# Performance work log

Hardware: AMD Instinct MI355X
Metric: run time of the kernel (lower is better)

The kernel has to match this reference:

```python
import jax, jax.numpy as jnp
import numpy as np

B, T, D = 16, 1024, 256
H, DK = 2, 128          # n_head, d_k = d_v = D // n_head
K = 5                   # conv kernel size
TEMP = float(np.sqrt(D))  # temperature = d_model ** 0.5


def mish(x):
    return x * jnp.tanh(jax.nn.softplus(x))


def setup_inputs() -> dict:
    key = jax.random.key(0)
    ks = jax.random.split(key, 16)
    s = 0.02
    p = lambda k, shp: jax.random.normal(k, shp, dtype=jnp.float32) * s
    inp = {
        'x': jax.random.normal(ks[0], (B, T, D), dtype=jnp.float32),
        'mask': jax.random.randint(ks[1], (B, T), 0, 2).astype(bool),
        # spectral MLP
        'W1': p(ks[2], (D, D)), 'b1': p(ks[3], (D,)),
        'W2': p(ks[4], (D, D)), 'b2': p(ks[5], (D,)),
        # two Conv1dGLU blocks: Conv1d(D -> 2D, k=5), torch layout [out,in,k]
        'cW1': p(ks[6], (2 * D, D, K)), 'cb1': p(ks[7], (2 * D,)),
        'cW2': p(ks[8], (2 * D, D, K)), 'cb2': p(ks[9], (2 * D,)),
        # attention projections (torch Linear: y = x @ W.T + b)
        'Wq': p(ks[10], (D, D)), 'bq': p(ks[11], (D,)),
        'Wk': p(ks[12], (D, D)), 'bk': p(ks[13], (D,)),
        'Wv': p(ks[14], (D, D)), 'bv': p(ks[15], (D,)),
        'Wo': p(jax.random.fold_in(key, 100), (D, D)),
        'bo': p(jax.random.fold_in(key, 101), (D,)),
        # final fc
        'Wf': p(jax.random.fold_in(key, 102), (D, D)),
        'bf': p(jax.random.fold_in(key, 103), (D,)),
    }
    return inp


def conv1d_glu(h, w, b):
    # h: [B, C, T]; w: [2C, C, K]; 'same' padding, GLU gate + residual
    y = jax.lax.conv_general_dilated(h, w, window_strides=(1,), padding=[(K // 2, K // 2)],
                                     dimension_numbers=('NCH', 'OIH', 'NCH'))
    y = y + b[None, :, None]
    a, g = jnp.split(y, 2, axis=1)
    return h + a * jax.nn.sigmoid(g)


def reference(x, mask, W1, b1, W2, b2, cW1, cb1, cW2, cb2,
              Wq, bq, Wk, bk, Wv, bv, Wo, bo, Wf, bf):
    # spectral: Linear + Mish (dropout is identity at inference)
    h = mish(x @ W1.T + b1)
    h = mish(h @ W2.T + b2)
    # temporal: two Conv1dGLU residual blocks over [B, C, T]
    h = h.transpose(0, 2, 1)
    h = conv1d_glu(h, cW1, cb1)
    h = conv1d_glu(h, cW2, cb2)
    h = h.transpose(0, 2, 1)
    # zero out padded frames
    h = jnp.where(mask[:, :, None], 0.0, h)
    residual = h
    # multi-head self-attention; mask hides padded keys
    q = (h @ Wq.T + bq).reshape(B, T, H, DK)
    k = (h @ Wk.T + bk).reshape(B, T, H, DK)
    v = (h @ Wv.T + bv).reshape(B, T, H, DK)
    attn = jnp.einsum('bqhd,bkhd->bhqk', q, k) / TEMP
    attn = jnp.where(mask[:, None, None, :], -jnp.inf, attn)
    attn = jax.nn.softmax(attn, axis=-1)
    out = jnp.einsum('bhqk,bkhd->bqhd', attn, v).reshape(B, T, D)
    h = out @ Wo.T + bo + residual
    # final projection + masked temporal average pool
    y = h @ Wf.T + bf
    len_ = (~mask).sum(axis=1, keepdims=True).astype(y.dtype)  # [B,1]
    y = jnp.where(mask[:, :, None], 0.0, y)
    w = y.sum(axis=1) / len_
    return w
```

## Files before the change

kernel.cpp:

```cpp
#include <hip/hip_runtime.h>
#include <hip/hip_bf16.h>
#include <math.h>


#define DEV __device__ __forceinline__

static constexpr int B_ = 16, T_ = 1024, D_ = 256;
static constexpr int N_ = B_ * T_;

typedef __attribute__((ext_vector_type(8))) short bf16x8;
typedef __attribute__((ext_vector_type(16))) float floatx16;

DEV float sigmoidf_(float x) { return 1.f / (1.f + __expf(-x)); }
DEV float mishf_(float x) {
  float u = __expf(fminf(x, 30.f));
  float t = u * (u + 2.f);
  return x * (t / (t + 2.f));
}
DEV ushort f2bf_(float x) {
  __hip_bfloat16 h = __float2bfloat16(x);
  return *(ushort*)&h;
}

__global__ __launch_bounds__(256) void prep_all_kernel(
    const float* __restrict__ x, const unsigned* __restrict__ mraw,
    const float* __restrict__ W1, const float* __restrict__ W2,
    const float* __restrict__ Wq, const float* __restrict__ Wk,
    const float* __restrict__ Wv, const float* __restrict__ Wo,
    const float* __restrict__ cW1, const float* __restrict__ cW2,
    ushort* __restrict__ G0, ushort* __restrict__ w1, ushort* __restrict__ w2,
    ushort* __restrict__ wqkv, ushort* __restrict__ wo,
    ushort* __restrict__ WtF1, ushort* __restrict__ WtF2,
    float* __restrict__ fmask, ushort* __restrict__ QE,
    ushort* __restrict__ KF, float* __restrict__ pooled) {
  int bid = blockIdx.x, tid = threadIdx.x;
  if (bid < 4096) {
    int i = bid * 256 + tid;
    float4 v = ((const float4*)x)[i];
    ushort4 u;
    u.x = f2bf_(v.x); u.y = f2bf_(v.y); u.z = f2bf_(v.z); u.w = f2bf_(v.w);
    ((ushort4*)G0)[i] = u;
  } else if (bid < 4480) {
    int i = (bid - 4096) * 256 + tid;
    int widx = i >> 14, r = i & 16383;
    const float* src;
    ushort* dst;
    switch (widx) {
      case 0: src = W1; dst = w1; break;
      case 1: src = W2; dst = w2; break;
      case 2: src = Wq; dst = wqkv; break;
      case 3: src = Wk; dst = wqkv + 65536; break;
      case 4: src = Wv; dst = wqkv + 131072; break;
      default: src = Wo; dst = wo; break;
    }
    float4 v = ((const float4*)src)[r];
    ushort4 u;
    u.x = f2bf_(v.x); u.y = f2bf_(v.y); u.z = f2bf_(v.z); u.w = f2bf_(v.w);
    ((ushort4*)dst)[r] = u;
  } else if (bid < 9600) {
    int idx = (bid - 4480) * 256 + tid;
    const float* cw = (idx < 655360) ? cW1 : cW2;
    ushort* dst = (idx < 655360) ? WtF1 : WtF2;
    int i = (idx < 655360) ? idx : idx - 655360;
    int j = i & 7, half = (i >> 3) & 1, m31 = (i >> 4) & 31;
    int frag = i >> 9;
    int ks = frag & 1, c = (frag >> 1) & 7, tap = (frag >> 4) % 5,
        cot = frag / 80;
    int co = cot * 32 + m31;
    int cin = c * 32 + ks * 16 + half * 8 + j;
    dst[i] = f2bf_(cw[(size_t)(co * 256 + cin) * 5 + tap]);
  } else {
    int isByte = 0, isFloat = 0;
    for (int i = 0; i < 16; ++i) {
      unsigned v = mraw[tid * 16 + i];
      if (v == 0x3F800000u) isFloat = 1;
      else if (v > 1u) isByte = 1;
    }
    __shared__ int sByte, sFloat;
    if (tid == 0) { sByte = 0; sFloat = 0; }
    __syncthreads();
    if (isByte) atomicOr(&sByte, 1);
    if (isFloat) atomicOr(&sFloat, 1);
    __syncthreads();
    int mode = sFloat ? 2 : (sByte ? 1 : 0);
    int mb = bid - 9600;
    int id = mb * 256 + tid;
    int bh = id >> 10, t = id & 1023, b = bh >> 1;
    int gidx = b * 1024 + t;
    unsigned mv;
    if (mode == 1) mv = ((const unsigned char*)mraw)[gidx];
    else           mv = mraw[gidx];
    float fm = (mv != 0u) ? 1.f : 0.f;
    if ((bh & 1) == 0) fmask[gidx] = fm;
    if (mb < 16) pooled[mb * 256 + tid] = 0.f;
    size_t qb = (size_t)id * 144 + 128;
    QE[qb] = f2bf_(1.f);
#pragma unroll
    for (int j = 1; j < 16; ++j) QE[qb + j] = 0;
    size_t kb = ((size_t)(bh * 32 + (t >> 5)) * 9 + 8) * 512 + (t & 31) * 16;
    KF[kb] = (fm != 0.f) ? f2bf_(-60000.f) : (ushort)0;
#pragma unroll
    for (int j = 1; j < 16; ++j) KF[kb + j] = 0;
  }
}

template <int ACT, int RESID, int OMODE>
__global__ __launch_bounds__(256, 2) void gemm_mfma_kernel(
    const ushort* __restrict__ A16, const ushort* __restrict__ W16,
    const float* __restrict__ bias, const float* __restrict__ resid,
    const float* __restrict__ fmask,
    float* __restrict__ outf, ushort* __restrict__ outb) {
  __shared__ __align__(16) ushort As[2][64 * 40];
  int tid = threadIdx.x;
  int w = tid >> 6, lane = tid & 63;
  int m31 = lane & 31, half = lane >> 5;
  int n0 = blockIdx.x * 64;

  floatx16 acc[2][2];
#pragma unroll
  for (int a = 0; a < 2; ++a)
#pragma unroll
    for (int b = 0; b < 2; ++b)
#pragma unroll
      for (int i = 0; i < 16; ++i) acc[a][b][i] = 0.f;

#pragma unroll
  for (int it = 0; it < 2; ++it) {
    int i = tid + it * 256;
    int row = i >> 3, part = i & 7;
    *(uint2*)&As[0][row * 40 + part * 4] =
        *(const uint2*)&A16[(size_t)(n0 + row) * 256 + part * 4];
  }
  bf16x8 bn[2][2];
#pragma unroll
  for (int ks = 0; ks < 2; ++ks)
#pragma unroll
    for (int ct = 0; ct < 2; ++ct)
      bn[ks][ct] = *(const bf16x8*)&W16[(size_t)(w * 64 + ct * 32 + m31) * 256 +
                                        ks * 16 + half * 8];

  for (int c = 0; c < 8; ++c) {
    __syncthreads();
    if (c < 7) {
      int k0 = (c + 1) * 32;
#pragma unroll
      for (int it = 0; it < 2; ++it) {
        int i = tid + it * 256;
        int row = i >> 3, part = i & 7;
        *(uint2*)&As[(c + 1) & 1][row * 40 + part * 4] =
            *(const uint2*)&A16[(size_t)(n0 + row) * 256 + k0 + part * 4];
      }
    }
    bf16x8 bc[2][2];
#pragma unroll
    for (int ks = 0; ks < 2; ++ks)
#pragma unroll
      for (int ct = 0; ct < 2; ++ct) bc[ks][ct] = bn[ks][ct];
    if (c < 7) {
      int k0 = (c + 1) * 32;
#pragma unroll
      for (int ks = 0; ks < 2; ++ks)
#pragma unroll
        for (int ct = 0; ct < 2; ++ct)
          bn[ks][ct] = *(const bf16x8*)&W16[
              (size_t)(w * 64 + ct * 32 + m31) * 256 + k0 + ks * 16 + half * 8];
    }
    const ushort* ab = As[c & 1];
#pragma unroll
    for (int ks = 0; ks < 2; ++ks) {
      bf16x8 af[2];
#pragma unroll
      for (int rt = 0; rt < 2; ++rt)
        af[rt] = *(const bf16x8*)&ab[(rt * 32 + m31) * 40 + ks * 16 + half * 8];
#pragma unroll
      for (int rt = 0; rt < 2; ++rt)
#pragma unroll
        for (int ct = 0; ct < 2; ++ct)
          acc[rt][ct] = __builtin_amdgcn_mfma_f32_32x32x16_bf16(
              af[rt], bc[ks][ct], acc[rt][ct], 0, 0, 0);
    }
  }
  if (OMODE == 3) {
    int b = n0 >> 10;
    float psum[2] = {0.f, 0.f};
    float bv0 = bias[w * 64 + m31], bv1 = bias[w * 64 + 32 + m31];
#pragma unroll
    for (int rt = 0; rt < 2; ++rt) {
#pragma unroll
      for (int reg = 0; reg < 16; ++reg) {
        int row = n0 + rt * 32 + (reg & 3) + 8 * (reg >> 2) + 4 * half;
        float keep = (fmask[row] == 0.f) ? 1.f : 0.f;
        float r0 = resid[(size_t)row * 256 + w * 64 + m31];
        float r1 = resid[(size_t)row * 256 + w * 64 + 32 + m31];
        psum[0] += keep * (acc[rt][0][reg] + bv0 + r0);
        psum[1] += keep * (acc[rt][1][reg] + bv1 + r1);
      }
    }
    atomicAdd(&outf[b * 256 + w * 64 + m31], psum[0]);
    atomicAdd(&outf[b * 256 + w * 64 + 32 + m31], psum[1]);
    return;
  }
#pragma unroll
  for (int ct = 0; ct < 2; ++ct) {
    int col = w * 64 + ct * 32 + m31;
    float bv = bias[col];
#pragma unroll
    for (int rt = 0; rt < 2; ++rt) {
#pragma unroll
      for (int reg = 0; reg < 16; ++reg) {
        int row = n0 + rt * 32 + (reg & 3) + 8 * (reg >> 2) + 4 * half;
        float v = acc[rt][ct][reg] + bv;
        if (ACT == 1) v = mishf_(v);
        if (RESID) v += resid[(size_t)row * 256 + col];
        if (OMODE == 0) {
          outf[(size_t)row * 256 + col] = v;
        } else if (OMODE == 1) {
          outb[(size_t)row * 256 + col] = f2bf_(v);
        } else {
          outf[(size_t)row * 256 + col] = v;
          outb[(size_t)row * 256 + col] = f2bf_(v);
        }
      }
    }
  }
}

__global__ __launch_bounds__(256, 2) void qkv_mfma_kernel(
    const ushort* __restrict__ A16, const ushort* __restrict__ wqkv,
    const float* __restrict__ bq, const float* __restrict__ bk,
    const float* __restrict__ bv,
    ushort* __restrict__ QE, ushort* __restrict__ KF, ushort* __restrict__ VF) {
  __shared__ __align__(16) ushort As[2][64 * 40];
  int tid = threadIdx.x;
  int w = tid >> 6, lane = tid & 63;
  int m31 = lane & 31, half = lane >> 5;
  int n0 = blockIdx.x * 64;
  int by = blockIdx.y;
  const ushort* W16 = wqkv + (size_t)by * 65536;
  const float* bias = (by == 0) ? bq : (by == 1) ? bk : bv;

  floatx16 acc[2][2];
#pragma unroll
  for (int a = 0; a < 2; ++a)
#pragma unroll
    for (int b = 0; b < 2; ++b)
#pragma unroll
      for (int i = 0; i < 16; ++i) acc[a][b][i] = 0.f;

#pragma unroll
  for (int it = 0; it < 2; ++it) {
    int i = tid + it * 256;
    int row = i >> 3, part = i & 7;
    *(uint2*)&As[0][row * 40 + part * 4] =
        *(const uint2*)&A16[(size_t)(n0 + row) * 256 + part * 4];
  }
  bf16x8 bn[2][2];
#pragma unroll
  for (int ks = 0; ks < 2; ++ks)
#pragma unroll
    for (int ct = 0; ct < 2; ++ct)
      bn[ks][ct] = *(const bf16x8*)&W16[(size_t)(w * 64 + ct * 32 + m31) * 256 +
                                        ks * 16 + half * 8];
  for (int c = 0; c < 8; ++c) {
    __syncthreads();
    if (c < 7) {
      int k0 = (c + 1) * 32;
#pragma unroll
      for (int it = 0; it < 2; ++it) {
        int i = tid + it * 256;
        int row = i >> 3, part = i & 7;
        *(uint2*)&As[(c + 1) & 1][row * 40 + part * 4] =
            *(const uint2*)&A16[(size_t)(n0 + row) * 256 + k0 + part * 4];
      }
    }
    bf16x8 bc[2][2];
#pragma unroll
    for (int ks = 0; ks < 2; ++ks)
#pragma unroll
      for (int ct = 0; ct < 2; ++ct) bc[ks][ct] = bn[ks][ct];
    if (c < 7) {
      int k0 = (c + 1) * 32;
#pragma unroll
      for (int ks = 0; ks < 2; ++ks)
#pragma unroll
        for (int ct = 0; ct < 2; ++ct)
          bn[ks][ct] = *(const bf16x8*)&W16[
              (size_t)(w * 64 + ct * 32 + m31) * 256 + k0 + ks * 16 + half * 8];
    }
    const ushort* ab = As[c & 1];
#pragma unroll
    for (int ks = 0; ks < 2; ++ks) {
      bf16x8 af[2];
#pragma unroll
      for (int rt = 0; rt < 2; ++rt)
        af[rt] = *(const bf16x8*)&ab[(rt * 32 + m31) * 40 + ks * 16 + half * 8];
#pragma unroll
      for (int rt = 0; rt < 2; ++rt)
#pragma unroll
        for (int ct = 0; ct < 2; ++ct)
          acc[rt][ct] = __builtin_amdgcn_mfma_f32_32x32x16_bf16(
              af[rt], bc[ks][ct], acc[rt][ct], 0, 0, 0);
    }
  }
  int b = n0 >> 10;
#pragma unroll
  for (int ct = 0; ct < 2; ++ct) {
    int col = w * 64 + ct * 32 + m31;
    float bvv = bias[col];
    int h = col >> 7, d127 = col & 127;
    int bh = b * 2 + h;
    if (by == 2) {
      int ctv = d127 >> 5, m31v = d127 & 31;
#pragma unroll
      for (int rt = 0; rt < 2; ++rt)
#pragma unroll
        for (int rg = 0; rg < 4; ++rg) {
          int t0 = (n0 & 1023) + rt * 32 + 8 * rg + 4 * half;
          ushort4 u;
          u.x = f2bf_(acc[rt][ct][rg * 4 + 0] + bvv);
          u.y = f2bf_(acc[rt][ct][rg * 4 + 1] + bvv);
          u.z = f2bf_(acc[rt][ct][rg * 4 + 2] + bvv);
          u.w = f2bf_(acc[rt][ct][rg * 4 + 3] + bvv);
          size_t addr = ((size_t)(bh * 16 + (t0 >> 6)) * 16 +
                         ((t0 >> 4) & 3) * 4 + ctv) * 512 +
                        m31v * 16 + ((t0 >> 3) & 1) * 8 + (t0 & 7);
          *(ushort4*)&VF[addr] = u;
        }
    } else {
#pragma unroll
      for (int rt = 0; rt < 2; ++rt)
#pragma unroll
        for (int reg = 0; reg < 16; ++reg) {
          int t = (n0 & 1023) + rt * 32 + (reg & 3) + 8 * (reg >> 2) + 4 * half;
          float v = acc[rt][ct][reg] + bvv;
          if (by == 0) {
            QE[((size_t)(bh * 1024 + t)) * 144 + d127] = f2bf_(v * 0.0625f);
          } else {
            size_t addr = ((size_t)(bh * 32 + (t >> 5)) * 9 + (d127 >> 4)) * 512 +
                          (t & 31) * 16 + ((d127 >> 3) & 1) * 8 + (d127 & 7);
            KF[addr] = f2bf_(v);
          }
        }
    }
  }
}

template <int DO_MASK>
__global__ __launch_bounds__(256, 2) void conv_mfma_kernel(
    const ushort* __restrict__ H16, const float* __restrict__ Hf,
    const ushort* __restrict__ WtF, const float* __restrict__ cb,
    const float* __restrict__ fmask, float* __restrict__ outf,
    ushort* __restrict__ outb) {
  __shared__ __align__(16) ushort As[2][132 * 40];
  int tid = threadIdx.x;
  int w = tid >> 6, lane = tid & 63;
  int m31 = lane & 31, half = lane >> 5;
  int wr = w >> 1, wc = w & 1;
  int cg = blockIdx.x;
  int n0 = blockIdx.y * 128;
  int tbase = n0 & 1023;
  int acol = cg * 64 + wc * 32;
  int cotA = cg * 2 + wc, cotG = 8 + cg * 2 + wc;

  floatx16 acc[2][2];
#pragma unroll
  for (int a = 0; a < 2; ++a)
#pragma unroll
    for (int b = 0; b < 2; ++b)
#pragma unroll
      for (int i = 0; i < 16; ++i) acc[a][b][i] = 0.f;

  for (int i = tid; i < 1056; i += 256) {
    int row = i >> 3, part = i & 7;
    int t = tbase + row - 2;
    uint2 v = make_uint2(0u, 0u);
    if ((unsigned)t < 1024u)
      v = *(const uint2*)&H16[(size_t)(n0 + row - 2) * 256 + part * 4];
    *(uint2*)&As[0][row * 40 + part * 4] = v;
  }
  bf16x8 bn[2][2];
#pragma unroll
  for (int ks = 0; ks < 2; ++ks) {
    bn[ks][0] = *(const bf16x8*)&WtF[(size_t)(((cotA * 5 + 0) * 8 + 0) * 2 + ks) * 512 +
                                     m31 * 16 + half * 8];
    bn[ks][1] = *(const bf16x8*)&WtF[(size_t)(((cotG * 5 + 0) * 8 + 0) * 2 + ks) * 512 +
                                     m31 * 16 + half * 8];
  }

  for (int c = 0; c < 8; ++c) {
    __syncthreads();
    if (c < 7) {
      int k0 = (c + 1) * 32;
      for (int i = tid; i < 1056; i += 256) {
        int row = i >> 3, part = i & 7;
        int t = tbase + row - 2;
        uint2 v = make_uint2(0u, 0u);
        if ((unsigned)t < 1024u)
          v = *(const uint2*)&H16[(size_t)(n0 + row - 2) * 256 + k0 + part * 4];
        *(uint2*)&As[(c + 1) & 1][row * 40 + part * 4] = v;
      }
    }
    const ushort* ab = As[c & 1];
#pragma unroll
    for (int tap = 0; tap < 5; ++tap) {
      bf16x8 bc[2][2];
#pragma unroll
      for (int ks = 0; ks < 2; ++ks)
#pragma unroll
        for (int ct = 0; ct < 2; ++ct) bc[ks][ct] = bn[ks][ct];
      int pc = c, pt = tap + 1;
      if (pt == 5) { pc = c + 1; pt = 0; }
      if (pc < 8) {
#pragma unroll
        for (int ks = 0; ks < 2; ++ks) {
          bn[ks][0] = *(const bf16x8*)&WtF[
              (size_t)(((cotA * 5 + pt) * 8 + pc) * 2 + ks) * 512 + m31 * 16 + half * 8];
          bn[ks][1] = *(const bf16x8*)&WtF[
              (size_t)(((cotG * 5 + pt) * 8 + pc) * 2 + ks) * 512 + m31 * 16 + half * 8];
        }
      }
#pragma unroll
      for (int ks = 0; ks < 2; ++ks) {
        bf16x8 af[2];
#pragma unroll
        for (int rt = 0; rt < 2; ++rt)
          af[rt] = *(const bf16x8*)&ab[(wr * 64 + rt * 32 + m31 + tap) * 40 +
                                       ks * 16 + half * 8];
#pragma unroll
        for (int rt = 0; rt < 2; ++rt)
#pragma unroll
          for (int ct = 0; ct < 2; ++ct)
            acc[rt][ct] = __builtin_amdgcn_mfma_f32_32x32x16_bf16(
                af[rt], bc[ks][ct], acc[rt][ct], 0, 0, 0);
      }
    }
  }
  int col = acol + m31;
  float ba = cb[col], bg = cb[256 + col];
#pragma unroll
  for (int rt = 0; rt < 2; ++rt) {
#pragma unroll
    for (int reg = 0; reg < 16; ++reg) {
      int brow = wr * 64 + rt * 32 + (reg & 3) + 8 * (reg >> 2) + 4 * half;
      int grow = n0 + brow;
      float a = acc[rt][0][reg] + ba;
      float g = acc[rt][1][reg] + bg;
      float v = Hf[(size_t)grow * 256 + col] + a * sigmoidf_(g);
      if (DO_MASK) {
        if (fmask[grow] != 0.f) v = 0.f;
      }
      outf[(size_t)grow * 256 + col] = v;
      outb[(size_t)grow * 256 + col] = f2bf_(v);
    }
  }
}

__global__ __launch_bounds__(256, 2) void attn_mfma2_kernel(
    const ushort* __restrict__ QE, const ushort* __restrict__ KF,
    const ushort* __restrict__ VF, ushort* __restrict__ O) {
  __shared__ float Op[2][128][33];
  __shared__ float Ml[2][2][32];
  int tid = threadIdx.x;
  int w = tid >> 6, lane = tid & 63;
  int m31 = lane & 31, half = lane >> 5;
  int qt = w & 1, kh = w >> 1;
  int bh = blockIdx.x;
  int q0 = blockIdx.y * 64 + qt * 32;
  int lpos = m31 * 16 + half * 8;

  bf16x8 qe[9];
  {
    size_t qrow = ((size_t)(bh * 1024 + q0 + m31)) * 144;
#pragma unroll
    for (int c = 0; c < 9; ++c)
      qe[c] = *(const bf16x8*)&QE[qrow + c * 16 + half * 8];
  }
  floatx16 oacc[4];
#pragma unroll
  for (int ct = 0; ct < 4; ++ct)
#pragma unroll
    for (int i = 0; i < 16; ++i) oacc[ct][i] = 0.f;
  float mi = -1e30f, li = 0.f;

  for (int it = 0; it < 8; ++it) {
    int ktb = kh * 512 + it * 64;
    int kfrag = (bh * 32 + (ktb >> 5)) * 9;
    int vtile = (bh * 16 + (ktb >> 6)) * 16;
    floatx16 s0, s1;
#pragma unroll
    for (int i = 0; i < 16; ++i) { s0[i] = 0.f; s1[i] = 0.f; }
#pragma unroll
    for (int c = 0; c < 9; ++c) {
      bf16x8 kf0 = *(const bf16x8*)&KF[(size_t)(kfrag + c) * 512 + lpos];
      bf16x8 kf1 = *(const bf16x8*)&KF[(size_t)(kfrag + 9 + c) * 512 + lpos];
      s0 = __builtin_amdgcn_mfma_f32_32x32x16_bf16(kf0, qe[c], s0, 0, 0, 0);
      s1 = __builtin_amdgcn_mfma_f32_32x32x16_bf16(kf1, qe[c], s1, 0, 0, 0);
    }
    bf16x8 vfr[2][4];
#pragma unroll
    for (int s2 = 0; s2 < 2; ++s2)
#pragma unroll
      for (int ct = 0; ct < 4; ++ct)
        vfr[s2][ct] = *(const bf16x8*)&VF[(size_t)(vtile + s2 * 4 + ct) * 512 + lpos];
    float mloc = s0[0];
#pragma unroll
    for (int r = 1; r < 16; ++r) mloc = fmaxf(mloc, s0[r]);
#pragma unroll
    for (int r = 0; r < 16; ++r) mloc = fmaxf(mloc, s1[r]);
    float mt = fmaxf(mloc, __shfl_xor(mloc, 32));
    float mnew = fmaxf(mi, mt);
    float alpha = __expf(mi - mnew);
    bool dead = (mnew <= -3.0e4f);
    float sum = 0.f;
#pragma unroll
    for (int r = 0; r < 16; ++r) {
      float v0 = dead ? 0.f : __expf(s0[r] - mnew);
      float v1 = dead ? 0.f : __expf(s1[r] - mnew);
      s0[r] = v0; s1[r] = v1;
      sum += v0 + v1;
    }
    sum += __shfl_xor(sum, 32);
    li = li * alpha + sum;
    mi = mnew;
#pragma unroll
    for (int ct = 0; ct < 4; ++ct)
#pragma unroll
      for (int i = 0; i < 16; ++i) oacc[ct][i] *= alpha;
    bf16x8 pf[4];
#pragma unroll
    for (int sub = 0; sub < 2; ++sub) {
      float tx[16];
#pragma unroll
      for (int r = 0; r < 16; ++r)
        tx[r] = __shfl_xor(sub == 0 ? s0[r] : s1[r], 32);
#pragma unroll
      for (int s = 0; s < 2; ++s) {
        union { bf16x8 v; ushort u[8]; } pk;
#pragma unroll
        for (int j = 0; j < 8; ++j) {
          int base = s * 8;
          float own = (sub == 0) ? s0[base + j] : s1[base + j];
          float lo = (j < 4) ? own : tx[base + j - 4];
          float hi = (j < 4) ? tx[base + 4 + j] : own;
          pk.u[j] = f2bf_(half ? hi : lo);
        }
        pf[sub * 2 + s] = pk.v;
      }
    }
#pragma unroll
    for (int s2 = 0; s2 < 4; ++s2)
#pragma unroll
      for (int ct = 0; ct < 4; ++ct) {
        bf16x8 vf = (s2 < 2) ? vfr[s2][ct]
                  : *(const bf16x8*)&VF[(size_t)(vtile + s2 * 4 + ct) * 512 + lpos];
        oacc[ct] = __builtin_amdgcn_mfma_f32_32x32x16_bf16(
            vf, pf[s2], oacc[ct], 0, 0, 0);
      }
  }
  if (kh == 1) {
#pragma unroll
    for (int ct = 0; ct < 4; ++ct)
#pragma unroll
      for (int r = 0; r < 16; ++r) {
        int dv = ct * 32 + (r & 3) + 8 * (r >> 2) + 4 * half;
        Op[qt][dv][m31] = oacc[ct][r];
      }
    if (half == 0) { Ml[qt][0][m31] = mi; Ml[qt][1][m31] = li; }
  }
  __syncthreads();
  if (kh == 0) {
    float mB = Ml[qt][0][m31], lB = Ml[qt][1][m31];
    float m = fmaxf(mi, mB);
    float aA = __expf(mi - m), aB = __expf(mB - m);
    float l = li * aA + lB * aB;
    float inv = (l > 0.f) ? 1.f / l : 0.f;
    int b = bh >> 1, h = bh & 1;
    size_t rowbase = (size_t)(b * 1024 + q0 + m31) * 256 + h * 128;
#pragma unroll
    for (int ct = 0; ct < 4; ++ct)
#pragma unroll
      for (int rg = 0; rg < 4; ++rg) {
        int dv0 = ct * 32 + 8 * rg + 4 * half;
        ushort4 u;
        u.x = f2bf_((oacc[ct][rg * 4 + 0] * aA + Op[qt][dv0 + 0][m31] * aB) * inv);
        u.y = f2bf_((oacc[ct][rg * 4 + 1] * aA + Op[qt][dv0 + 1][m31] * aB) * inv);
        u.z = f2bf_((oacc[ct][rg * 4 + 2] * aA + Op[qt][dv0 + 2][m31] * aB) * inv);
        u.w = f2bf_((oacc[ct][rg * 4 + 3] * aA + Op[qt][dv0 + 3][m31] * aB) * inv);
        *(ushort4*)&O[rowbase + dv0] = u;
      }
  }
}

__global__ __launch_bounds__(256) void final_kernel(
    const float* __restrict__ pooled, const float* __restrict__ fmask,
    const float* __restrict__ Wf, const float* __restrict__ bf,
    float* __restrict__ out) {
  int b = blockIdx.x, j = threadIdx.x;
  __shared__ __align__(16) float p[256];
  __shared__ float red[256];
  p[j] = pooled[b * 256 + j];
  float c = 0.f;
  for (int i = 0; i < 4; ++i)
    c += (fmask[b * 1024 + i * 256 + j] == 0.f) ? 1.f : 0.f;
  red[j] = c;
  __syncthreads();
  for (int st = 128; st > 0; st >>= 1) {
    if (j < st) red[j] += red[j + st];
    __syncthreads();
  }
  float len = red[0];
  const float* wrow = Wf + (size_t)j * 256;
  float acc = 0.f;
  for (int d4 = 0; d4 < 64; ++d4) {
    float4 wv = ((const float4*)wrow)[d4];
    float4 pv = ((const float4*)p)[d4];
    acc += wv.x * pv.x + wv.y * pv.y + wv.z * pv.z + wv.w * pv.w;
  }
  float inv = (len > 0.f) ? 1.f / len : 0.f;
  out[b * 256 + j] = acc * inv + bf[j];
}

extern "C" void kernel_launch(void* const* d_in, const int* in_sizes, int n_in,
                              void* d_out, int out_size, void* d_ws, size_t ws_size,
                              hipStream_t stream) {
  const float* x      = (const float*)d_in[0];
  const unsigned* msk = (const unsigned*)d_in[1];
  const float* W1 = (const float*)d_in[2];
  const float* b1 = (const float*)d_in[3];
  const float* W2 = (const float*)d_in[4];
  const float* b2 = (const float*)d_in[5];
  const float* cW1 = (const float*)d_in[6];
  const float* cb1 = (const float*)d_in[7];
  const float* cW2 = (const float*)d_in[8];
  const float* cb2 = (const float*)d_in[9];
  const float* Wq = (const float*)d_in[10];
  const float* bq = (const float*)d_in[11];
  const float* Wk = (const float*)d_in[12];
  const float* bk = (const float*)d_in[13];
  const float* Wv = (const float*)d_in[14];
  const float* bv = (const float*)d_in[15];
  const float* Wo = (const float*)d_in[16];
  const float* bo = (const float*)d_in[17];
  const float* Wf = (const float*)d_in[18];
  const float* bf = (const float*)d_in[19];
  float* out = (float*)d_out;

  float* ws = (float*)d_ws;
  size_t ND = (size_t)N_ * D_;
  float* F0      = ws;
  float* F1      = F0 + ND;
  float* fmask   = F1 + ND;
  float* pooled  = fmask + N_;
  ushort* G0 = (ushort*)(pooled + 16 * 256);
  ushort* G1 = G0 + ND;
  ushort* QE = G1 + ND;
  ushort* KF = QE + (size_t)32 * 1024 * 144;
  ushort* VF = KF + (size_t)32 * 32 * 9 * 512;
  ushort* w1_16 = VF + (size_t)32 * 16 * 16 * 512;
  ushort* w2_16 = w1_16 + 65536;
  ushort* wo_16 = w2_16 + 65536;
  ushort* wqkv  = wo_16 + 65536;
  ushort* WtF1  = wqkv + 3 * 65536;
  ushort* WtF2  = WtF1 + 655360;

  dim3 blk(256);
  prep_all_kernel<<<dim3(9728), blk, 0, stream>>>(
      x, msk, W1, W2, Wq, Wk, Wv, Wo, cW1, cW2,
      G0, w1_16, w2_16, wqkv, wo_16, WtF1, WtF2, fmask, QE, KF, pooled);
  gemm_mfma_kernel<1, 0, 1><<<dim3(256), blk, 0, stream>>>(
      G0, w1_16, b1, nullptr, nullptr, nullptr, G1);
  gemm_mfma_kernel<1, 0, 2><<<dim3(256), blk, 0, stream>>>(
      G1, w2_16, b2, nullptr, nullptr, F0, G0);
  conv_mfma_kernel<0><<<dim3(4, 128), blk, 0, stream>>>(
      G0, F0, WtF1, cb1, fmask, F1, G1);
  conv_mfma_kernel<1><<<dim3(4, 128), blk, 0, stream>>>(
      G1, F1, WtF2, cb2, fmask, F0, G0);
  qkv_mfma_kernel<<<dim3(256, 3), blk, 0, stream>>>(
      G0, wqkv, bq, bk, bv, QE, KF, VF);
  attn_mfma2_kernel<<<dim3(32, 16), blk, 0, stream>>>(QE, KF, VF, G1);
  gemm_mfma_kernel<0, 1, 3><<<dim3(256), blk, 0, stream>>>(
      G1, wo_16, bo, F0, fmask, pooled, nullptr);
  final_kernel<<<dim3(16), blk, 0, stream>>>(pooled, fmask, Wf, bf, out);
}
```

Measured before the change: 327.6 us.

## Shrink per-block tiles to launch more blocks across GEMM, conv and attention kernels

Every GEMM, QKV, conv and attention kernel is repartitioned into smaller tiles so each launch has many more blocks. GEMMs go from 64x256 to 32x128 output tiles, conv from 128 to 64 time rows, and attention now splits the key range four ways per 32-query tile with a two-stage softmax merge. The goal is to fill more of the many CUs on the device and raise occupancy through the launch bounds. The cost is less data reuse per block, more redundant A and W loads, and extra LDS synchronisation in the attention merge.

Result: slower. 368.6 us (+12.5%).

```diff
diff --git a/kernel.cpp b/kernel.cpp
--- a/kernel.cpp
+++ b/kernel.cpp
@@ -105,272 +105,194 @@
 }
 
 template <int ACT, int RESID, int OMODE>
-__global__ __launch_bounds__(256, 2) void gemm_mfma_kernel(
+__global__ __launch_bounds__(256, 4) void gemm_mfma_kernel(
     const ushort* __restrict__ A16, const ushort* __restrict__ W16,
     const float* __restrict__ bias, const float* __restrict__ resid,
     const float* __restrict__ fmask,
     float* __restrict__ outf, ushort* __restrict__ outb) {
-  __shared__ __align__(16) ushort As[2][64 * 40];
+  __shared__ __align__(16) ushort As[2][32 * 40];
   int tid = threadIdx.x;
   int w = tid >> 6, lane = tid & 63;
   int m31 = lane & 31, half = lane >> 5;
-  int n0 = blockIdx.x * 64;
-
-  floatx16 acc[2][2];
-#pragma unroll
-  for (int a = 0; a < 2; ++a)
-#pragma unroll
-    for (int b = 0; b < 2; ++b)
-#pragma unroll
-      for (int i = 0; i < 16; ++i) acc[a][b][i] = 0.f;
-
-#pragma unroll
-  for (int it = 0; it < 2; ++it) {
-    int i = tid + it * 256;
-    int row = i >> 3, part = i & 7;
+  int n0 = blockIdx.x * 32;
+  int col = blockIdx.y * 128 + w * 32 + m31;
+
+  floatx16 acc;
+#pragma unroll
+  for (int i = 0; i < 16; ++i) acc[i] = 0.f;
+
+  {
+    int row = tid >> 3, part = tid & 7;
     *(uint2*)&As[0][row * 40 + part * 4] =
         *(const uint2*)&A16[(size_t)(n0 + row) * 256 + part * 4];
   }
-  bf16x8 bn[2][2];
+  bf16x8 bn[2];
 #pragma unroll
   for (int ks = 0; ks < 2; ++ks)
-#pragma unroll
-    for (int ct = 0; ct < 2; ++ct)
-      bn[ks][ct] = *(const bf16x8*)&W16[(size_t)(w * 64 + ct * 32 + m31) * 256 +
-                                        ks * 16 + half * 8];
+    bn[ks] = *(const bf16x8*)&W16[(size_t)col * 256 + ks * 16 + half * 8];
 
   for (int c = 0; c < 8; ++c) {
     __syncthreads();
     if (c < 7) {
       int k0 = (c + 1) * 32;
-#pragma unroll
-      for (int it = 0; it < 2; ++it) {
-        int i = tid + it * 256;
-        int row = i >> 3, part = i & 7;
-        *(uint2*)&As[(c + 1) & 1][row * 40 + part * 4] =
-            *(const uint2*)&A16[(size_t)(n0 + row) * 256 + k0 + part * 4];
-      }
-    }
-    bf16x8 bc[2][2];
-#pragma unroll
-    for (int ks = 0; ks < 2; ++ks)
-#pragma unroll
-      for (int ct = 0; ct < 2; ++ct) bc[ks][ct] = bn[ks][ct];
+      int row = tid >> 3, part = tid & 7;
+      *(uint2*)&As[(c + 1) & 1][row * 40 + part * 4] =
+          *(const uint2*)&A16[(size_t)(n0 + row) * 256 + k0 + part * 4];
+    }
+    bf16x8 bc[2] = {bn[0], bn[1]};
     if (c < 7) {
       int k0 = (c + 1) * 32;
 #pragma unroll
       for (int ks = 0; ks < 2; ++ks)
-#pragma unroll
-        for (int ct = 0; ct < 2; ++ct)
-          bn[ks][ct] = *(const bf16x8*)&W16[
-              (size_t)(w * 64 + ct * 32 + m31) * 256 + k0 + ks * 16 + half * 8];
+        bn[ks] = *(const bf16x8*)&W16[(size_t)col * 256 + k0 + ks * 16 + half * 8];
     }
     const ushort* ab = As[c & 1];
 #pragma unroll
     for (int ks = 0; ks < 2; ++ks) {
-      bf16x8 af[2];
-#pragma unroll
-      for (int rt = 0; rt < 2; ++rt)
-        af[rt] = *(const bf16x8*)&ab[(rt * 32 + m31) * 40 + ks * 16 + half * 8];
-#pragma unroll
-      for (int rt = 0; rt < 2; ++rt)
-#pragma unroll
-        for (int ct = 0; ct < 2; ++ct)
-          acc[rt][ct] = __builtin_amdgcn_mfma_f32_32x32x16_bf16(
-              af[rt], bc[ks][ct], acc[rt][ct], 0, 0, 0);
-    }
-  }
+      bf16x8 af = *(const bf16x8*)&ab[m31 * 40 + ks * 16 + half * 8];
+      acc = __builtin_amdgcn_mfma_f32_32x32x16_bf16(af, bc[ks], acc, 0, 0, 0);
+    }
+  }
+  float bv = bias[col];
   if (OMODE == 3) {
     int b = n0 >> 10;
-    float psum[2] = {0.f, 0.f};
-    float bv0 = bias[w * 64 + m31], bv1 = bias[w * 64 + 32 + m31];
-#pragma unroll
-    for (int rt = 0; rt < 2; ++rt) {
-#pragma unroll
-      for (int reg = 0; reg < 16; ++reg) {
-        int row = n0 + rt * 32 + (reg & 3) + 8 * (reg >> 2) + 4 * half;
-        float keep = (fmask[row] == 0.f) ? 1.f : 0.f;
-        float r0 = resid[(size_t)row * 256 + w * 64 + m31];
-        float r1 = resid[(size_t)row * 256 + w * 64 + 32 + m31];
-        psum[0] += keep * (acc[rt][0][reg] + bv0 + r0);
-        psum[1] += keep * (acc[rt][1][reg] + bv1 + r1);
-      }
-    }
-    atomicAdd(&outf[b * 256 + w * 64 + m31], psum[0]);
-    atomicAdd(&outf[b * 256 + w * 64 + 32 + m31], psum[1]);
+    float psum = 0.f;
+#pragma unroll
+    for (int reg = 0; reg < 16; ++reg) {
+      int row = n0 + (reg & 3) + 8 * (reg >> 2) + 4 * half;
+      float keep = (fmask[row] == 0.f) ? 1.f : 0.f;
+      psum += keep * (acc[reg] + bv + resid[(size_t)row * 256 + col]);
+    }
+    atomicAdd(&outf[b * 256 + col], psum);
     return;
   }
 #pragma unroll
-  for (int ct = 0; ct < 2; ++ct) {
-    int col = w * 64 + ct * 32 + m31;
-    float bv = bias[col];
-#pragma unroll
-    for (int rt = 0; rt < 2; ++rt) {
-#pragma unroll
-      for (int reg = 0; reg < 16; ++reg) {
-        int row = n0 + rt * 32 + (reg & 3) + 8 * (reg >> 2) + 4 * half;
-        float v = acc[rt][ct][reg] + bv;
-        if (ACT == 1) v = mishf_(v);
-        if (RESID) v += resid[(size_t)row * 256 + col];
-        if (OMODE == 0) {
-          outf[(size_t)row * 256 + col] = v;
-        } else if (OMODE == 1) {
-          outb[(size_t)row * 256 + col] = f2bf_(v);
-        } else {
-          outf[(size_t)row * 256 + col] = v;
-          outb[(size_t)row * 256 + col] = f2bf_(v);
-        }
-      }
-    }
-  }
-}
-
-__global__ __launch_bounds__(256, 2) void qkv_mfma_kernel(
+  for (int reg = 0; reg < 16; ++reg) {
+    int row = n0 + (reg & 3) + 8 * (reg >> 2) + 4 * half;
+    float v = acc[reg] + bv;
+    if (ACT == 1) v = mishf_(v);
+    if (RESID) v += resid[(size_t)row * 256 + col];
+    if (OMODE == 0) {
+      outf[(size_t)row * 256 + col] = v;
+    } else if (OMODE == 1) {
+      outb[(size_t)row * 256 + col] = f2bf_(v);
+    } else {
+      outf[(size_t)row * 256 + col] = v;
+      outb[(size_t)row * 256 + col] = f2bf_(v);
+    }
+  }
+}
+
+__global__ __launch_bounds__(256, 4) void qkv_mfma_kernel(
     const ushort* __restrict__ A16, const ushort* __restrict__ wqkv,
     const float* __restrict__ bq, const float* __restrict__ bk,
     const float* __restrict__ bv,
     ushort* __restrict__ QE, ushort* __restrict__ KF, ushort* __restrict__ VF) {
-  __shared__ __align__(16) ushort As[2][64 * 40];
+  __shared__ __align__(16) ushort As[2][32 * 40];
   int tid = threadIdx.x;
   int w = tid >> 6, lane = tid & 63;
   int m31 = lane & 31, half = lane >> 5;
-  int n0 = blockIdx.x * 64;
-  int by = blockIdx.y;
+  int n0 = blockIdx.x * 32;
+  int by = blockIdx.z;
   const ushort* W16 = wqkv + (size_t)by * 65536;
   const float* bias = (by == 0) ? bq : (by == 1) ? bk : bv;
-
-  floatx16 acc[2][2];
-#pragma unroll
-  for (int a = 0; a < 2; ++a)
-#pragma unroll
-    for (int b = 0; b < 2; ++b)
-#pragma unroll
-      for (int i = 0; i < 16; ++i) acc[a][b][i] = 0.f;
-
-#pragma unroll
-  for (int it = 0; it < 2; ++it) {
-    int i = tid + it * 256;
-    int row = i >> 3, part = i & 7;
+  int col = blockIdx.y * 128 + w * 32 + m31;
+
+  floatx16 acc;
+#pragma unroll
+  for (int i = 0; i < 16; ++i) acc[i] = 0.f;
+
+  {
+    int row = tid >> 3, part = tid & 7;
     *(uint2*)&As[0][row * 40 + part * 4] =
         *(const uint2*)&A16[(size_t)(n0 + row) * 256 + part * 4];
   }
-  bf16x8 bn[2][2];
+  bf16x8 bn[2];
 #pragma unroll
   for (int ks = 0; ks < 2; ++ks)
-#pragma unroll
-    for (int ct = 0; ct < 2; ++ct)
-      bn[ks][ct] = *(const bf16x8*)&W16[(size_t)(w * 64 + ct * 32 + m31) * 256 +
-                                        ks * 16 + half * 8];
+    bn[ks] = *(const bf16x8*)&W16[(size_t)col * 256 + ks * 16 + half * 8];
+
   for (int c = 0; c < 8; ++c) {
     __syncthreads();
     if (c < 7) {
       int k0 = (c + 1) * 32;
-#pragma unroll
-      for (int it = 0; it < 2; ++it) {
-        int i = tid + it * 256;
-        int row = i >> 3, part = i & 7;
-        *(uint2*)&As[(c + 1) & 1][row * 40 + part * 4] =
-            *(const uint2*)&A16[(size_t)(n0 + row) * 256 + k0 + part * 4];
-      }
-    }
-    bf16x8 bc[2][2];
-#pragma unroll
-    for (int ks = 0; ks < 2; ++ks)
-#pragma unroll
-      for (int ct = 0; ct < 2; ++ct) bc[ks][ct] = bn[ks][ct];
+      int row = tid >> 3, part = tid & 7;
+      *(uint2*)&As[(c + 1) & 1][row * 40 + part * 4] =
+          *(const uint2*)&A16[(size_t)(n0 + row) * 256 + k0 + part * 4];
+    }
+    bf16x8 bc[2] = {bn[0], bn[1]};
     if (c < 7) {
       int k0 = (c + 1) * 32;
 #pragma unroll
       for (int ks = 0; ks < 2; ++ks)
-#pragma unroll
-        for (int ct = 0; ct < 2; ++ct)
-          bn[ks][ct] = *(const bf16x8*)&W16[
-              (size_t)(w * 64 + ct * 32 + m31) * 256 + k0 + ks * 16 + half * 8];
+        bn[ks] = *(const bf16x8*)&W16[(size_t)col * 256 + k0 + ks * 16 + half * 8];
     }
     const ushort* ab = As[c & 1];
 #pragma unroll
     for (int ks = 0; ks < 2; ++ks) {
-      bf16x8 af[2];
-#pragma unroll
-      for (int rt = 0; rt < 2; ++rt)
-        af[rt] = *(const bf16x8*)&ab[(rt * 32 + m31) * 40 + ks * 16 + half * 8];
-#pragma unroll
-      for (int rt = 0; rt < 2; ++rt)
-#pragma unroll
-        for (int ct = 0; ct < 2; ++ct)
-          acc[rt][ct] = __builtin_amdgcn_mfma_f32_32x32x16_bf16(
-              af[rt], bc[ks][ct], acc[rt][ct], 0, 0, 0);
+      bf16x8 af = *(const bf16x8*)&ab[m31 * 40 + ks * 16 + half * 8];
+      acc = __builtin_amdgcn_mfma_f32_32x32x16_bf16(af, bc[ks], acc, 0, 0, 0);
     }
   }
   int b = n0 >> 10;
-#pragma unroll
-  for (int ct = 0; ct < 2; ++ct) {
-    int col = w * 64 + ct * 32 + m31;
-    float bvv = bias[col];
-    int h = col >> 7, d127 = col & 127;
-    int bh = b * 2 + h;
-    if (by == 2) {
-      int ctv = d127 >> 5, m31v = d127 & 31;
-#pragma unroll
-      for (int rt = 0; rt < 2; ++rt)
-#pragma unroll
-        for (int rg = 0; rg < 4; ++rg) {
-          int t0 = (n0 & 1023) + rt * 32 + 8 * rg + 4 * half;
-          ushort4 u;
-          u.x = f2bf_(acc[rt][ct][rg * 4 + 0] + bvv);
-          u.y = f2bf_(acc[rt][ct][rg * 4 + 1] + bvv);
-          u.z = f2bf_(acc[rt][ct][rg * 4 + 2] + bvv);
-          u.w = f2bf_(acc[rt][ct][rg * 4 + 3] + bvv);
-          size_t addr = ((size_t)(bh * 16 + (t0 >> 6)) * 16 +
-                         ((t0 >> 4) & 3) * 4 + ctv) * 512 +
-                        m31v * 16 + ((t0 >> 3) & 1) * 8 + (t0 & 7);
-          *(ushort4*)&VF[addr] = u;
-        }
-    } else {
-#pragma unroll
-      for (int rt = 0; rt < 2; ++rt)
-#pragma unroll
-        for (int reg = 0; reg < 16; ++reg) {
-          int t = (n0 & 1023) + rt * 32 + (reg & 3) + 8 * (reg >> 2) + 4 * half;
-          float v = acc[rt][ct][reg] + bvv;
-          if (by == 0) {
-            QE[((size_t)(bh * 1024 + t)) * 144 + d127] = f2bf_(v * 0.0625f);
-          } else {
-            size_t addr = ((size_t)(bh * 32 + (t >> 5)) * 9 + (d127 >> 4)) * 512 +
-                          (t & 31) * 16 + ((d127 >> 3) & 1) * 8 + (d127 & 7);
-            KF[addr] = f2bf_(v);
-          }
-        }
+  float bvv = bias[col];
+  int h = col >> 7, d127 = col & 127;
+  int bh = b * 2 + h;
+  if (by == 2) {
+    int ctv = d127 >> 5, m31v = d127 & 31;
+#pragma unroll
+    for (int rg = 0; rg < 4; ++rg) {
+      int t0 = (n0 & 1023) + 8 * rg + 4 * half;
+      ushort4 u;
+      u.x = f2bf_(acc[rg * 4 + 0] + bvv);
+      u.y = f2bf_(acc[rg * 4 + 1] + bvv);
+      u.z = f2bf_(acc[rg * 4 + 2] + bvv);
+      u.w = f2bf_(acc[rg * 4 + 3] + bvv);
+      size_t addr = ((size_t)(bh * 16 + (t0 >> 6)) * 16 +
+                     ((t0 >> 4) & 3) * 4 + ctv) * 512 +
+                    m31v * 16 + ((t0 >> 3) & 1) * 8 + (t0 & 7);
+      *(ushort4*)&VF[addr] = u;
+    }
+  } else {
+#pragma unroll
+    for (int reg = 0; reg < 16; ++reg) {
+      int t = (n0 & 1023) + (reg & 3) + 8 * (reg >> 2) + 4 * half;
+      float v = acc[reg] + bvv;
+      if (by == 0) {
+        QE[((size_t)(bh * 1024 + t)) * 144 + d127] = f2bf_(v * 0.0625f);
+      } else {
+        size_t addr = ((size_t)(bh * 32 + (t >> 5)) * 9 + (d127 >> 4)) * 512 +
+                      (t & 31) * 16 + ((d127 >> 3) & 1) * 8 + (d127 & 7);
+        KF[addr] = f2bf_(v);
+      }
     }
   }
 }
 
 template <int DO_MASK>
-__global__ __launch_bounds__(256, 2) void conv_mfma_kernel(
+__global__ __launch_bounds__(256, 3) void conv_mfma_kernel(
     const ushort* __restrict__ H16, const float* __restrict__ Hf,
     const ushort* __restrict__ WtF, const float* __restrict__ cb,
     const float* __restrict__ fmask, float* __restrict__ outf,
     ushort* __restrict__ outb) {
-  __shared__ __align__(16) ushort As[2][132 * 40];
+  __shared__ __align__(16) ushort As[2][68 * 40];
   int tid = threadIdx.x;
   int w = tid >> 6, lane = tid & 63;
   int m31 = lane & 31, half = lane >> 5;
   int wr = w >> 1, wc = w & 1;
-  int cg = blockIdx.x;
-  int n0 = blockIdx.y * 128;
+  int n0 = blockIdx.x * 64;
+  int cg = blockIdx.y;
   int tbase = n0 & 1023;
   int acol = cg * 64 + wc * 32;
   int cotA = cg * 2 + wc, cotG = 8 + cg * 2 + wc;
 
-  floatx16 acc[2][2];
-#pragma unroll
-  for (int a = 0; a < 2; ++a)
-#pragma unroll
-    for (int b = 0; b < 2; ++b)
-#pragma unroll
-      for (int i = 0; i < 16; ++i) acc[a][b][i] = 0.f;
-
-  for (int i = tid; i < 1056; i += 256) {
+  floatx16 acc[2];
+#pragma unroll
+  for (int ct = 0; ct < 2; ++ct)
+#pragma unroll
+    for (int i = 0; i < 16; ++i) acc[ct][i] = 0.f;
+
+  for (int i = tid; i < 544; i += 256) {
     int row = i >> 3, part = i & 7;
     int t = tbase + row - 2;
     uint2 v = make_uint2(0u, 0u);
@@ -391,7 +313,7 @@
     __syncthreads();
     if (c < 7) {
       int k0 = (c + 1) * 32;
-      for (int i = tid; i < 1056; i += 256) {
+      for (int i = tid; i < 544; i += 256) {
         int row = i >> 3, part = i & 7;
         int t = tbase + row - 2;
         uint2 v = make_uint2(0u, 0u);
@@ -421,41 +343,33 @@
       }
 #pragma unroll
       for (int ks = 0; ks < 2; ++ks) {
-        bf16x8 af[2];
-#pragma unroll
-        for (int rt = 0; rt < 2; ++rt)
-          af[rt] = *(const bf16x8*)&ab[(wr * 64 + rt * 32 + m31 + tap) * 40 +
-                                       ks * 16 + half * 8];
-#pragma unroll
-        for (int rt = 0; rt < 2; ++rt)
-#pragma unroll
-          for (int ct = 0; ct < 2; ++ct)
-            acc[rt][ct] = __builtin_amdgcn_mfma_f32_32x32x16_bf16(
-                af[rt], bc[ks][ct], acc[rt][ct], 0, 0, 0);
+        bf16x8 af = *(const bf16x8*)&ab[(wr * 32 + m31 + tap) * 40 +
+                                        ks * 16 + half * 8];
+#pragma unroll
+        for (int ct = 0; ct < 2; ++ct)
+          acc[ct] = __builtin_amdgcn_mfma_f32_32x32x16_bf16(
+              af, bc[ks][ct], acc[ct], 0, 0, 0);
       }
     }
   }
   int col = acol + m31;
   float ba = cb[col], bg = cb[256 + col];
 #pragma unroll
-  for (int rt = 0; rt < 2; ++rt) {
-#pragma unroll
-    for (int reg = 0; reg < 16; ++reg) {
-      int brow = wr * 64 + rt * 32 + (reg & 3) + 8 * (reg >> 2) + 4 * half;
-      int grow = n0 + brow;
-      float a = acc[rt][0][reg] + ba;
-      float g = acc[rt][1][reg] + bg;
-      float v = Hf[(size_t)grow * 256 + col] + a * sigmoidf_(g);
-      if (DO_MASK) {
-        if (fmask[grow] != 0.f) v = 0.f;
-      }
-      outf[(size_t)grow * 256 + col] = v;
-      outb[(size_t)grow * 256 + col] = f2bf_(v);
-    }
-  }
-}
-
-__global__ __launch_bounds__(256, 2) void attn_mfma2_kernel(
+  for (int reg = 0; reg < 16; ++reg) {
+    int brow = wr * 32 + (reg & 3) + 8 * (reg >> 2) + 4 * half;
+    int grow = n0 + brow;
+    float a = acc[0][reg] + ba;
+    float g = acc[1][reg] + bg;
+    float v = Hf[(size_t)grow * 256 + col] + a * sigmoidf_(g);
+    if (DO_MASK) {
+      if (fmask[grow] != 0.f) v = 0.f;
+    }
+    outf[(size_t)grow * 256 + col] = v;
+    outb[(size_t)grow * 256 + col] = f2bf_(v);
+  }
+}
+
+__global__ __launch_bounds__(256, 3) void attn_mfma3_kernel(
     const ushort* __restrict__ QE, const ushort* __restrict__ KF,
     const ushort* __restrict__ VF, ushort* __restrict__ O) {
   __shared__ float Op[2][128][33];
@@ -463,9 +377,8 @@
   int tid = threadIdx.x;
   int w = tid >> 6, lane = tid & 63;
   int m31 = lane & 31, half = lane >> 5;
-  int qt = w & 1, kh = w >> 1;
   int bh = blockIdx.x;
-  int q0 = blockIdx.y * 64 + qt * 32;
+  int q0 = blockIdx.y * 32;
   int lpos = m31 * 16 + half * 8;
 
   bf16x8 qe[9];
@@ -482,8 +395,8 @@
     for (int i = 0; i < 16; ++i) oacc[ct][i] = 0.f;
   float mi = -1e30f, li = 0.f;
 
-  for (int it = 0; it < 8; ++it) {
-    int ktb = kh * 512 + it * 64;
+  for (int it = 0; it < 4; ++it) {
+    int ktb = w * 256 + it * 64;
     int kfrag = (bh * 32 + (ktb >> 5)) * 9;
     int vtile = (bh * 16 + (ktb >> 6)) * 16;
     floatx16 s0, s1;
@@ -557,19 +470,45 @@
             vf, pf[s2], oacc[ct], 0, 0, 0);
       }
   }
-  if (kh == 1) {
+  if (w >= 2) {
 #pragma unroll
     for (int ct = 0; ct < 4; ++ct)
 #pragma unroll
       for (int r = 0; r < 16; ++r) {
         int dv = ct * 32 + (r & 3) + 8 * (r >> 2) + 4 * half;
-        Op[qt][dv][m31] = oacc[ct][r];
-      }
-    if (half == 0) { Ml[qt][0][m31] = mi; Ml[qt][1][m31] = li; }
+        Op[w - 2][dv][m31] = oacc[ct][r];
+      }
+    if (half == 0) { Ml[w - 2][0][m31] = mi; Ml[w - 2][1][m31] = li; }
   }
   __syncthreads();
-  if (kh == 0) {
-    float mB = Ml[qt][0][m31], lB = Ml[qt][1][m31];
+  if (w < 2) {
+    float mB = Ml[w][0][m31], lB = Ml[w][1][m31];
+    float m = fmaxf(mi, mB);
+    float aA = __expf(mi - m), aB = __expf(mB - m);
+    li = li * aA + lB * aB;
+    mi = m;
+#pragma unroll
+    for (int ct = 0; ct < 4; ++ct)
+#pragma unroll
+      for (int r = 0; r < 16; ++r) {
+        int dv = ct * 32 + (r & 3) + 8 * (r >> 2) + 4 * half;
+        oacc[ct][r] = oacc[ct][r] * aA + Op[w][dv][m31] * aB;
+      }
+  }
+  __syncthreads();
+  if (w == 1) {
+#pragma unroll
+    for (int ct = 0; ct < 4; ++ct)
+#pragma unroll
+      for (int r = 0; r < 16; ++r) {
+        int dv = ct * 32 + (r & 3) + 8 * (r >> 2) + 4 * half;
+        Op[0][dv][m31] = oacc[ct][r];
+      }
+    if (half == 0) { Ml[0][0][m31] = mi; Ml[0][1][m31] = li; }
+  }
+  __syncthreads();
+  if (w == 0) {
+    float mB = Ml[0][0][m31], lB = Ml[0][1][m31];
     float m = fmaxf(mi, mB);
     float aA = __expf(mi - m), aB = __expf(mB - m);
     float l = li * aA + lB * aB;
@@ -582,10 +521,10 @@
       for (int rg = 0; rg < 4; ++rg) {
         int dv0 = ct * 32 + 8 * rg + 4 * half;
         ushort4 u;
-        u.x = f2bf_((oacc[ct][rg * 4 + 0] * aA + Op[qt][dv0 + 0][m31] * aB) * inv);
-        u.y = f2bf_((oacc[ct][rg * 4 + 1] * aA + Op[qt][dv0 + 1][m31] * aB) * inv);
-        u.z = f2bf_((oacc[ct][rg * 4 + 2] * aA + Op[qt][dv0 + 2][m31] * aB) * inv);
-        u.w = f2bf_((oacc[ct][rg * 4 + 3] * aA + Op[qt][dv0 + 3][m31] * aB) * inv);
+        u.x = f2bf_((oacc[ct][rg * 4 + 0] * aA + Op[0][dv0 + 0][m31] * aB) * inv);
+        u.y = f2bf_((oacc[ct][rg * 4 + 1] * aA + Op[0][dv0 + 1][m31] * aB) * inv);
+        u.z = f2bf_((oacc[ct][rg * 4 + 2] * aA + Op[0][dv0 + 2][m31] * aB) * inv);
+        u.w = f2bf_((oacc[ct][rg * 4 + 3] * aA + Op[0][dv0 + 3][m31] * aB) * inv);
         *(ushort4*)&O[rowbase + dv0] = u;
       }
   }
@@ -667,18 +606,18 @@
   prep_all_kernel<<<dim3(9728), blk, 0, stream>>>(
       x, msk, W1, W2, Wq, Wk, Wv, Wo, cW1, cW2,
       G0, w1_16, w2_16, wqkv, wo_16, WtF1, WtF2, fmask, QE, KF, pooled);
-  gemm_mfma_kernel<1, 0, 1><<<dim3(256), blk, 0, stream>>>(
+  gemm_mfma_kernel<1, 0, 1><<<dim3(512, 2), blk, 0, stream>>>(
       G0, w1_16, b1, nullptr, nullptr, nullptr, G1);
-  gemm_mfma_kernel<1, 0, 2><<<dim3(256), blk, 0, stream>>>(
+  gemm_mfma_kernel<1, 0, 2><<<dim3(512, 2), blk, 0, stream>>>(
       G1, w2_16, b2, nullptr, nullptr, F0, G0);
-  conv_mfma_kernel<0><<<dim3(4, 128), blk, 0, stream>>>(
+  conv_mfma_kernel<0><<<dim3(256, 4), blk, 0, stream>>>(
       G0, F0, WtF1, cb1, fmask, F1, G1);
-  conv_mfma_kernel<1><<<dim3(4, 128), blk, 0, stream>>>(
+  conv_mfma_kernel<1><<<dim3(256, 4), blk, 0, stream>>>(
       G1, F1, WtF2, cb2, fmask, F0, G0);
-  qkv_mfma_kernel<<<dim3(256, 3), blk, 0, stream>>>(
+  qkv_mfma_kernel<<<dim3(512, 2, 3), blk, 0, stream>>>(
       G0, wqkv, bq, bk, bv, QE, KF, VF);
-  attn_mfma2_kernel<<<dim3(32, 16), blk, 0, stream>>>(QE, KF, VF, G1);
-  gemm_mfma_kernel<0, 1, 3><<<dim3(256), blk, 0, stream>>>(
+  attn_mfma3_kernel<<<dim3(32, 32), blk, 0, stream>>>(QE, KF, VF, G1);
+  gemm_mfma_kernel<0, 1, 3><<<dim3(512, 2), blk, 0, stream>>>(
       G1, wo_16, bo, F0, fmask, pooled, nullptr);
   final_kernel<<<dim3(16), blk, 0, stream>>>(pooled, fmask, Wf, bf, out);
 }
```
